# Optimization experiments

Measured on AMD Instinct MI355X. Metric: run time of the kernel, lower is better.

## Reference

```python
import jax, jax.numpy as jnp
import numpy as np

B, IN, H, N_FRAMES = 256, 1024, 2048, 32
BN_EPS = 1e-5


def setup_inputs() -> dict:
    key = jax.random.key(0)
    ks = jax.random.split(key, 10)
    s_in = 1.0 / np.sqrt(IN)
    s_h = 1.0 / np.sqrt(H)
    return {
        "x": jax.random.normal(ks[0], (B, IN), jnp.float32),
        "W_x": jax.random.normal(ks[1], (IN, 3 * H), jnp.float32) * s_in,
        "W_h": jax.random.normal(ks[2], (H, 3 * H), jnp.float32) * s_h,
        "b_x": jnp.zeros((3 * H,), jnp.float32),
        "b_h": jnp.zeros((3 * H,), jnp.float32),
        "W_d": jax.random.normal(ks[3], (H, IN), jnp.float32) * s_h,
        "b_d": jnp.zeros((IN,), jnp.float32),
        "gamma": jnp.ones((IN,), jnp.float32),
        "beta": jnp.zeros((IN,), jnp.float32),
        "n_frames": N_FRAMES,
    }


def reference(x, W_x, W_h, b_x, b_h, W_d, b_d, gamma, beta, n_frames):
    Bsz = x.shape[0]
    Hh = W_h.shape[0]
    h0 = jnp.zeros((Bsz, Hh), x.dtype)

    def step(carry, _):
        h, inp = carry
        gx = inp @ W_x + b_x                      # [B, 3H]
        gh = h @ W_h + b_h                        # [B, 3H]
        xr, xz, xn = jnp.split(gx, 3, axis=-1)
        hr, hz, hn = jnp.split(gh, 3, axis=-1)
        r = jax.nn.sigmoid(xr + hr)
        z = jax.nn.sigmoid(xz + hz)
        n = jnp.tanh(xn + r * hn)
        h_new = (1.0 - z) * n + z * h             # GRU update
        out = h_new @ W_d + b_d                   # fed back as next input
        return (h_new, out), out

    _, outs = jax.lax.scan(step, (h0, x), None, length=n_frames)  # [T, B, IN]
    # BatchNorm1d applied per frame over the batch dim (training-mode stats)
    mean = jnp.mean(outs, axis=1, keepdims=True)
    var = jnp.var(outs, axis=1, keepdims=True)
    return (outs - mean) * jax.lax.rsqrt(var + BN_EPS) * gamma + beta
```

## Files before the change

### kernel.cpp

```cpp
#include <hip/hip_runtime.h>
#include <hip/hip_bf16.h>
#include <stdint.h>


typedef __attribute__((ext_vector_type(8))) _Float16 half8;
typedef __attribute__((ext_vector_type(4))) float f32x4;
typedef unsigned short u16;

#define GLB_CAST(p) ((const __attribute__((address_space(1))) void*)(p))
#define LDS_CAST(p) ((__attribute__((address_space(3))) void*)(p))

static __device__ __forceinline__ void gload_lds16(const void* g, void* l) {
  __builtin_amdgcn_global_load_lds(GLB_CAST(g), LDS_CAST(l), 16, 0, 0);
}
static __device__ __forceinline__ u16 f2h(float f) {
  _Float16 h = (_Float16)f;
  return __builtin_bit_cast(u16, h);
}
static __device__ __forceinline__ float h2f(u16 u) {
  _Float16 h = __builtin_bit_cast(_Float16, u);
  return (float)h;
}

__global__ __launch_bounds__(256) void transpose_conv(
    const float* __restrict__ src, int src_ld, int j0,
    u16* __restrict__ dst, int dst_ld)
{
  __shared__ float tile[32][33];
  const int kt = blockIdx.y * 32, jt = blockIdx.x * 32;
  const int tr = threadIdx.x >> 5, tc = threadIdx.x & 31;
#pragma unroll
  for (int r = 0; r < 4; r++)
    tile[tr + r * 8][tc] = src[(size_t)(kt + tr + r * 8) * src_ld + j0 + jt + tc];
  __syncthreads();
#pragma unroll
  for (int r = 0; r < 4; r++)
    dst[(size_t)(jt + tr + r * 8) * dst_ld + kt + tc] = f2h(tile[tc][tr + r * 8]);
}

__global__ __launch_bounds__(256) void convert_f2h(
    const float* __restrict__ src, u16* __restrict__ dst)
{
  const int i = (blockIdx.x * 256 + threadIdx.x) * 4;
  float4 v = *(const float4*)(src + i);
  dst[i + 0] = f2h(v.x); dst[i + 1] = f2h(v.y);
  dst[i + 2] = f2h(v.z); dst[i + 3] = f2h(v.w);
}

__global__ __launch_bounds__(256) void bconst_kernel(
    const float* __restrict__ bx, const float* __restrict__ bd,
    const u16* __restrict__ XT, float* __restrict__ bc)
{
  __shared__ float sbd[1024];
  const int tid = threadIdx.x;
  for (int i = tid; i < 1024; i += 256) sbd[i] = bd[i];
  __syncthreads();
  const int j = blockIdx.x * 256 + tid;
  const u16* row = XT + (size_t)j * 1024;
  float s = bx[j];
  for (int k = 0; k < 1024; k += 8) {
    half8 v = *(const half8*)(row + k);
#pragma unroll
    for (int u = 0; u < 8; u++) s += sbd[k + u] * (float)v[u];
  }
  bc[j] = s;
}

template <int EPI>
__global__ __launch_bounds__(256) void gemm128_kernel(
    const u16* __restrict__ A, int lda,
    const u16* __restrict__ Bm, int ldb,
    int K, int ldc,
    u16* __restrict__ Cw, const u16* __restrict__ HT,
    float* __restrict__ Cf, const float* __restrict__ bias)
{
  __shared__ __attribute__((aligned(16))) u16 a_lds[128 * 64];
  __shared__ __attribute__((aligned(16))) u16 b_lds[128 * 64];
  const int tid = threadIdx.x, w = tid >> 6, l = tid & 63;
  const int rw = w >> 1, jw = w & 1;
  const int m0 = blockIdx.x * 128, n0 = blockIdx.y * 128;

  f32x4 acc[4][4] = {};

  for (int kk = 0; kk < K; kk += 64) {
    __syncthreads();
#pragma unroll
    for (int rnd = 0; rnd < 4; rnd++) {
      int flat = rnd * 256 + tid;
      int row = flat >> 3, gch = (flat & 7) ^ (row & 7);
      gload_lds16(A + (size_t)(m0 + row) * lda + kk + gch * 8, a_lds + flat * 8);
      gload_lds16(Bm + (size_t)(n0 + row) * ldb + kk + gch * 8, b_lds + flat * 8);
    }
    __syncthreads();
#pragma unroll
    for (int kh = 0; kh < 2; kh++) {
      const int koff = kh * 4 + (l >> 4);
      half8 a[4], b[4];
#pragma unroll
      for (int mf = 0; mf < 4; mf++) {
        int arow = rw * 64 + mf * 16 + (l & 15);
        a[mf] = *(const half8*)(a_lds + (arow * 8 + (koff ^ (arow & 7))) * 8);
      }
#pragma unroll
      for (int nf = 0; nf < 4; nf++) {
        int brow = jw * 64 + nf * 16 + (l & 15);
        b[nf] = *(const half8*)(b_lds + (brow * 8 + (koff ^ (brow & 7))) * 8);
      }
#pragma unroll
      for (int mf = 0; mf < 4; mf++)
#pragma unroll
        for (int nf = 0; nf < 4; nf++)
          acc[mf][nf] = __builtin_amdgcn_mfma_f32_16x16x32_f16(a[mf], b[nf], acc[mf][nf], 0, 0, 0);
    }
  }

#pragma unroll
  for (int mf = 0; mf < 4; mf++)
#pragma unroll
    for (int nf = 0; nf < 4; nf++) {
      const int n = n0 + jw * 64 + nf * 16 + (l & 15);
#pragma unroll
      for (int i = 0; i < 4; i++) {
        const int m = m0 + rw * 64 + mf * 16 + (l >> 4) * 4 + i;
        float v = acc[mf][nf][i];
        if (EPI == 0) {
          if (m < 4096) v += h2f(HT[(size_t)m * 2048 + n]);
          Cw[(size_t)m * ldc + n] = f2h(v);
        } else {
          Cf[(size_t)m * ldc + n] = v + bias[n];
        }
      }
    }
}

__global__ __launch_bounds__(512) void frame0_kernel(
    const u16* __restrict__ x16, const u16* __restrict__ XT,
    const float* __restrict__ bx, const float* __restrict__ bh,
    float* __restrict__ h32out, u16* __restrict__ hout16)
{
  __shared__ __attribute__((aligned(16))) u16 a_lds[2][64 * 64];
  __shared__ __attribute__((aligned(16))) u16 b_lds[2][96 * 64];
  const int tid = threadIdx.x, w = tid >> 6, l = tid & 63;
  const int rw = w >> 1, jw = w & 1;
  const int jt = blockIdx.x, r0 = blockIdx.y * 64;
  f32x4 acc[3] = {};

  const int ar = tid >> 3;
  const int agch = (tid & 7) ^ (ar & 7);
  const u16* asrc = x16 + (size_t)(r0 + ar) * 1024 + agch * 8;
  const u16* bsrc0;
  const u16* bsrc1;
  {
    int row0 = tid >> 3, gch0 = (tid & 7) ^ (row0 & 7);
    bsrc0 = XT + (size_t)((row0 >> 5) * 2048 + jt * 32 + (row0 & 31)) * 1024 + gch0 * 8;
    int flat = 512 + tid;
    int row1 = flat >> 3, gch1 = (flat & 7) ^ (row1 & 7);
    bsrc1 = XT + (size_t)((row1 >> 5) * 2048 + jt * 32 + (row1 & 31)) * 1024 + gch1 * 8;
  }

  auto stage = [&](int buf, int kk) {
    gload_lds16(asrc + kk, a_lds[buf] + tid * 8);
    gload_lds16(bsrc0 + kk, b_lds[buf] + tid * 8);
    if (512 + tid < 768)
      gload_lds16(bsrc1 + kk, b_lds[buf] + (512 + tid) * 8);
  };

  stage(0, 0);
  __syncthreads();
  int cur = 0;
  for (int t = 0; t < 16; ++t) {
    if (t < 15) stage(cur ^ 1, (t + 1) * 64);
    const int arow = rw * 16 + (l & 15);
#pragma unroll
    for (int kh = 0; kh < 2; kh++) {
      int apch = (kh * 4 + (l >> 4)) ^ (arow & 7);
      half8 a = *(const half8*)(a_lds[cur] + arow * 64 + apch * 8);
#pragma unroll
      for (int s = 0; s < 3; s++) {
        int brow = s * 32 + jw * 16 + (l & 15);
        int bpch = (kh * 4 + (l >> 4)) ^ (brow & 7);
        half8 bf = *(const half8*)(b_lds[cur] + brow * 64 + bpch * 8);
        acc[s] = __builtin_amdgcn_mfma_f32_16x16x32_f16(a, bf, acc[s], 0, 0, 0);
      }
    }
    __syncthreads();
    cur ^= 1;
  }

  const int j = jt * 32 + jw * 16 + (l & 15);
  const float cR = bx[j] + bh[j];
  const float cZ = bx[2048 + j] + bh[2048 + j];
  const float cX = bx[4096 + j];
  const float hn0 = bh[4096 + j];
#pragma unroll
  for (int i = 0; i < 4; i++) {
    const int b = r0 + rw * 16 + (l >> 4) * 4 + i;
    float r = 1.f / (1.f + __expf(-(acc[0][i] + cR)));
    float z = 1.f / (1.f + __expf(-(acc[1][i] + cZ)));
    float n = tanhf(acc[2][i] + cX + r * hn0);
    float hv = (1.f - z) * n;
    h32out[b * 2048 + j] = hv;
    hout16[b * 2048 + j] = f2h(hv);
  }
}

__global__ __launch_bounds__(512) void frame_kernel(
    const u16* __restrict__ hin16,
    const u16* __restrict__ WC,
    const float* __restrict__ bc, const float* __restrict__ bh,
    const float* __restrict__ h32in, float* __restrict__ h32out,
    u16* __restrict__ hout16)
{
  __shared__ __attribute__((aligned(16))) u16 a_lds[4][64 * 64];
  __shared__ __attribute__((aligned(16))) u16 b_lds[4][128 * 64];
  const int tid = threadIdx.x, w = tid >> 6, l = tid & 63;
  const int rw = (w >> 2) & 1, jw = (w >> 1) & 1, kw = w & 1;
  const int jt = blockIdx.x, r0 = blockIdx.y * 64;

  f32x4 acc[2][4] = {};

  const int ar = tid >> 3, agch = (tid & 7) ^ (ar & 7);
  const u16* asrc = hin16 + (size_t)(r0 + ar) * 2048 + agch * 8;
  const u16* bsrc0;
  const u16* bsrc1;
  {
    int row0 = tid >> 3, gch0 = (tid & 7) ^ (row0 & 7);
    bsrc0 = WC + (size_t)((row0 >> 5) * 2048 + jt * 32 + (row0 & 31)) * 2048 + gch0 * 8;
    int flat = 512 + tid;
    int row1 = flat >> 3, gch1 = (flat & 7) ^ (row1 & 7);
    bsrc1 = WC + (size_t)((row1 >> 5) * 2048 + jt * 32 + (row1 & 31)) * 2048 + gch1 * 8;
  }

  auto stage = [&](int buf, int step) {
    const int kk = step * 64;
    gload_lds16(asrc + kk, a_lds[buf] + tid * 8);
    gload_lds16(bsrc0 + kk, b_lds[buf] + tid * 8);
    gload_lds16(bsrc1 + kk, b_lds[buf] + (512 + tid) * 8);
  };

  auto compute = [&](int buf) {
    const int koff = kw * 4 + (l >> 4);
    half8 a[2], b[4];
#pragma unroll
    for (int mf = 0; mf < 2; mf++) {
      int arow = rw * 32 + mf * 16 + (l & 15);
      a[mf] = *(const half8*)(a_lds[buf] + (arow * 8 + (koff ^ (arow & 7))) * 8);
    }
#pragma unroll
    for (int s = 0; s < 4; s++) {
      int brow = s * 32 + jw * 16 + (l & 15);
      b[s] = *(const half8*)(b_lds[buf] + (brow * 8 + (koff ^ (brow & 7))) * 8);
    }
    __builtin_amdgcn_s_setprio(1);
#pragma unroll
    for (int mf = 0; mf < 2; mf++)
#pragma unroll
      for (int s = 0; s < 4; s++)
        acc[mf][s] = __builtin_amdgcn_mfma_f32_16x16x32_f16(a[mf], b[s], acc[mf][s], 0, 0, 0);
    __builtin_amdgcn_s_setprio(0);
  };

  stage(0, 0);
  stage(1, 1);
#pragma unroll 1
  for (int t = 0; t < 30; ++t) {
    stage((t + 2) & 3, t + 2);
    asm volatile("s_waitcnt vmcnt(6)\n\ts_barrier" ::: "memory");
    compute(t & 3);
  }
  asm volatile("s_waitcnt vmcnt(3)\n\ts_barrier" ::: "memory");
  compute(30 & 3);
  asm volatile("s_waitcnt vmcnt(0)\n\ts_barrier" ::: "memory");
  compute(31 & 3);

  __syncthreads();
  float* xch = (float*)&a_lds[0][0];
  const int wid2 = rw * 2 + jw;
  if (kw == 1) {
#pragma unroll
    for (int mf = 0; mf < 2; mf++)
#pragma unroll
      for (int s = 0; s < 4; s++)
        *(f32x4*)(xch + ((((wid2 * 2 + mf) * 4 + s) * 64 + l) * 4)) = acc[mf][s];
  }
  __syncthreads();
  if (kw == 0) {
#pragma unroll
    for (int mf = 0; mf < 2; mf++)
#pragma unroll
      for (int s = 0; s < 4; s++) {
        f32x4 p = *(const f32x4*)(xch + ((((wid2 * 2 + mf) * 4 + s) * 64 + l) * 4));
        acc[mf][s] += p;
      }
    const int j = jt * 32 + jw * 16 + (l & 15);
    const float cR = bc[j] + bh[j];
    const float cZ = bc[2048 + j] + bh[2048 + j];
    const float cX = bc[4096 + j];
    const float cH = bh[4096 + j];
#pragma unroll
    for (int mf = 0; mf < 2; mf++)
#pragma unroll
      for (int i = 0; i < 4; i++) {
        const int b = r0 + rw * 32 + mf * 16 + (l >> 4) * 4 + i;
        float r = 1.f / (1.f + __expf(-(acc[mf][0][i] + cR)));
        float z = 1.f / (1.f + __expf(-(acc[mf][1][i] + cZ)));
        float n = tanhf(acc[mf][2][i] + cX + r * (acc[mf][3][i] + cH));
        float hp = h32in[b * 2048 + j];
        float hv = (1.f - z) * n + z * hp;
        h32out[b * 2048 + j] = hv;
        hout16[b * 2048 + j] = f2h(hv);
      }
  }
}

__global__ __launch_bounds__(256) void bn_kernel(
    float* __restrict__ O, const float* __restrict__ gamma,
    const float* __restrict__ beta)
{
  const int t = blockIdx.x, j = blockIdx.y * 256 + threadIdx.x;
  const size_t base = (size_t)t * 256 * 1024 + j;
  float s = 0.f, q = 0.f;
  for (int b = 0; b < 256; b++) {
    float v = O[base + (size_t)b * 1024];
    s += v; q += v * v;
  }
  const float mean = s * (1.f / 256.f);
  const float var = q * (1.f / 256.f) - mean * mean;
  const float inv = rsqrtf(var + 1e-5f);
  const float g = gamma[j] * inv, be = beta[j];
  for (int b = 0; b < 256; b++) {
    const size_t idx = base + (size_t)b * 1024;
    O[idx] = (O[idx] - mean) * g + be;
  }
}

extern "C" void kernel_launch(void* const* d_in, const int* in_sizes, int n_in,
                              void* d_out, int out_size, void* d_ws, size_t ws_size,
                              hipStream_t stream)
{
  (void)in_sizes; (void)n_in; (void)out_size; (void)ws_size;
  const float* x  = (const float*)d_in[0];
  const float* Wx = (const float*)d_in[1];
  const float* Wh = (const float*)d_in[2];
  const float* bx = (const float*)d_in[3];
  const float* bh = (const float*)d_in[4];
  const float* Wd = (const float*)d_in[5];
  const float* bd = (const float*)d_in[6];
  const float* gamma = (const float*)d_in[7];
  const float* beta  = (const float*)d_in[8];

  char* p = (char*)d_ws;
  u16* XT  = (u16*)p;  p += (size_t)6144 * 1024 * 2;
  u16* WC  = (u16*)p;  p += (size_t)8192 * 2048 * 2;
  u16* DT  = (u16*)p;  p += (size_t)1024 * 2048 * 2;
  float* h32a = (float*)p; p += (size_t)256 * 2048 * 4;
  float* h32b = (float*)p; p += (size_t)256 * 2048 * 4;
  u16* x16 = (u16*)p;  p += (size_t)256 * 1024 * 2;
  float* bc = (float*)p; p += (size_t)6144 * 4;
  u16* Hs   = (u16*)p;
  u16* HT   = (u16*)p;
  u16* Wd16 = (u16*)(p + (size_t)4096 * 2048 * 2);

  const size_t BH = (size_t)256 * 2048;

  transpose_conv<<<dim3(192, 32), 256, 0, stream>>>(Wx, 6144, 0, XT, 1024);
  transpose_conv<<<dim3(128, 64), 256, 0, stream>>>(Wh, 6144, 0, HT, 2048);
  transpose_conv<<<dim3(64, 64), 256, 0, stream>>>(Wh, 6144, 4096,
                                                   WC + (size_t)6144 * 2048, 2048);
  transpose_conv<<<dim3(32, 64), 256, 0, stream>>>(Wd, 1024, 0, DT, 2048);
  convert_f2h<<<2048, 256, 0, stream>>>(Wd, Wd16);
  convert_f2h<<<256, 256, 0, stream>>>(x, x16);
  bconst_kernel<<<24, 256, 0, stream>>>(bx, bd, XT, bc);
  gemm128_kernel<0><<<dim3(48, 16), 256, 0, stream>>>(
      XT, 1024, Wd16, 1024, 1024, 2048, WC, HT, nullptr, nullptr);

  frame0_kernel<<<dim3(64, 4), 512, 0, stream>>>(x16, XT, bx, bh, h32a, Hs);
  for (int t = 1; t < 32; t++) {
    const float* hin32 = (t & 1) ? h32a : h32b;
    float* hout32      = (t & 1) ? h32b : h32a;
    frame_kernel<<<dim3(64, 4), 512, 0, stream>>>(
        Hs + (size_t)(t - 1) * BH, WC, bc, bh, hin32, hout32, Hs + (size_t)t * BH);
  }

  gemm128_kernel<1><<<dim3(64, 8), 256, 0, stream>>>(
      Hs, 2048, DT, 2048, 2048, 1024, nullptr, nullptr, (float*)d_out, bd);
  bn_kernel<<<dim3(32, 4), 256, 0, stream>>>((float*)d_out, gamma, beta);
}
```

Before: 810.7 us.

## Double-buffer GEMMs, widen frame K-step, fuse BN stats into output GEMM

The generic gemm128 kernel is split into two specialised 512-thread kernels, each with double-buffered LDS staging driven by explicit vmcnt waits. The output GEMM uses a wider 256-column tile and accumulates per-frame BatchNorm sum and sum-of-squares through shuffles and atomics, so the BN pass only reads the output once to normalise it. The recurrent frame kernel moves from a 4-deep 64-wide K pipeline to a 2-deep 128-wide K pipeline, halving the loop trip count and the number of barriers. The cost is larger LDS footprint and float atomics whose summation order is not deterministic.

Result: slower. 879.2 us (+8.4%).

```diff
diff --git a/kernel.cpp b/kernel.cpp
--- a/kernel.cpp
+++ b/kernel.cpp
@@ -66,45 +66,134 @@
   bc[j] = s;
 }
 
-template <int EPI>
-__global__ __launch_bounds__(256) void gemm128_kernel(
-    const u16* __restrict__ A, int lda,
-    const u16* __restrict__ Bm, int ldb,
-    int K, int ldc,
-    u16* __restrict__ Cw, const u16* __restrict__ HT,
-    float* __restrict__ Cf, const float* __restrict__ bias)
-{
-  __shared__ __attribute__((aligned(16))) u16 a_lds[128 * 64];
-  __shared__ __attribute__((aligned(16))) u16 b_lds[128 * 64];
+__global__ __launch_bounds__(512) void gemm_wc(
+    const u16* __restrict__ A, const u16* __restrict__ Bm,
+    const u16* __restrict__ HT, u16* __restrict__ Cw)
+{
+  __shared__ __attribute__((aligned(16))) u16 a_lds[2][128 * 64];
+  __shared__ __attribute__((aligned(16))) u16 b_lds[2][128 * 64];
   const int tid = threadIdx.x, w = tid >> 6, l = tid & 63;
   const int rw = w >> 1, jw = w & 1;
   const int m0 = blockIdx.x * 128, n0 = blockIdx.y * 128;
-
+  f32x4 acc[2][4] = {};
+
+  const u16 *asrc[2], *bsrc[2];
+#pragma unroll
+  for (int rnd = 0; rnd < 2; rnd++) {
+    int flat = rnd * 512 + tid;
+    int row = flat >> 3, gch = (flat & 7) ^ (row & 7);
+    asrc[rnd] = A + (size_t)(m0 + row) * 1024 + gch * 8;
+    bsrc[rnd] = Bm + (size_t)(n0 + row) * 1024 + gch * 8;
+  }
+  auto stage = [&](int buf, int kk) {
+#pragma unroll
+    for (int rnd = 0; rnd < 2; rnd++) {
+      int flat = rnd * 512 + tid;
+      gload_lds16(asrc[rnd] + kk, a_lds[buf] + flat * 8);
+      gload_lds16(bsrc[rnd] + kk, b_lds[buf] + flat * 8);
+    }
+  };
+  auto compute = [&](int buf) {
+    __builtin_amdgcn_s_setprio(1);
+#pragma unroll
+    for (int kh = 0; kh < 2; kh++) {
+      const int c = kh * 4 + (l >> 4);
+      half8 a[2], b[4];
+#pragma unroll
+      for (int mf = 0; mf < 2; mf++) {
+        int arow = rw * 32 + mf * 16 + (l & 15);
+        a[mf] = *(const half8*)(a_lds[buf] + (arow * 8 + (c ^ (arow & 7))) * 8);
+      }
+#pragma unroll
+      for (int nf = 0; nf < 4; nf++) {
+        int brow = jw * 64 + nf * 16 + (l & 15);
+        b[nf] = *(const half8*)(b_lds[buf] + (brow * 8 + (c ^ (brow & 7))) * 8);
+      }
+#pragma unroll
+      for (int mf = 0; mf < 2; mf++)
+#pragma unroll
+        for (int nf = 0; nf < 4; nf++)
+          acc[mf][nf] = __builtin_amdgcn_mfma_f32_16x16x32_f16(a[mf], b[nf], acc[mf][nf], 0, 0, 0);
+    }
+    __builtin_amdgcn_s_setprio(0);
+  };
+
+  stage(0, 0);
+#pragma unroll 1
+  for (int t = 0; t < 16; ++t) {
+    if (t < 15) {
+      stage((t + 1) & 1, (t + 1) * 64);
+      asm volatile("s_waitcnt vmcnt(4)\ns_barrier" ::: "memory");
+    } else {
+      asm volatile("s_waitcnt vmcnt(0)\ns_barrier" ::: "memory");
+    }
+    compute(t & 1);
+    asm volatile("s_barrier" ::: "memory");
+  }
+
+#pragma unroll
+  for (int mf = 0; mf < 2; mf++)
+#pragma unroll
+    for (int nf = 0; nf < 4; nf++) {
+      const int n = n0 + jw * 64 + nf * 16 + (l & 15);
+#pragma unroll
+      for (int i = 0; i < 4; i++) {
+        const int m = m0 + rw * 32 + mf * 16 + (l >> 4) * 4 + i;
+        float v = acc[mf][nf][i];
+        if (m < 4096) v += h2f(HT[(size_t)m * 2048 + n]);
+        Cw[(size_t)m * 2048 + n] = f2h(v);
+      }
+    }
+}
+
+__global__ __launch_bounds__(512) void gemm_out(
+    const u16* __restrict__ A, const u16* __restrict__ Bm,
+    const float* __restrict__ bd, float* __restrict__ O,
+    float* __restrict__ bnsum, float* __restrict__ bnsq)
+{
+  __shared__ __attribute__((aligned(16))) u16 a_lds[2][128 * 64];
+  __shared__ __attribute__((aligned(16))) u16 b_lds[2][256 * 64];
+  const int tid = threadIdx.x, w = tid >> 6, l = tid & 63;
+  const int rw = w >> 2, jw = w & 3;
+  const int m0 = blockIdx.x * 128, n0 = blockIdx.y * 256;
   f32x4 acc[4][4] = {};
 
-  for (int kk = 0; kk < K; kk += 64) {
-    __syncthreads();
-#pragma unroll
-    for (int rnd = 0; rnd < 4; rnd++) {
-      int flat = rnd * 256 + tid;
-      int row = flat >> 3, gch = (flat & 7) ^ (row & 7);
-      gload_lds16(A + (size_t)(m0 + row) * lda + kk + gch * 8, a_lds + flat * 8);
-      gload_lds16(Bm + (size_t)(n0 + row) * ldb + kk + gch * 8, b_lds + flat * 8);
-    }
-    __syncthreads();
+  const u16 *asrc[2], *bsrc[4];
+#pragma unroll
+  for (int rnd = 0; rnd < 2; rnd++) {
+    int flat = rnd * 512 + tid;
+    int row = flat >> 3, gch = (flat & 7) ^ (row & 7);
+    asrc[rnd] = A + (size_t)(m0 + row) * 2048 + gch * 8;
+  }
+#pragma unroll
+  for (int rnd = 0; rnd < 4; rnd++) {
+    int flat = rnd * 512 + tid;
+    int row = flat >> 3, gch = (flat & 7) ^ (row & 7);
+    bsrc[rnd] = Bm + (size_t)(n0 + row) * 2048 + gch * 8;
+  }
+  auto stage = [&](int buf, int kk) {
+#pragma unroll
+    for (int rnd = 0; rnd < 2; rnd++)
+      gload_lds16(asrc[rnd] + kk, a_lds[buf] + (rnd * 512 + tid) * 8);
+#pragma unroll
+    for (int rnd = 0; rnd < 4; rnd++)
+      gload_lds16(bsrc[rnd] + kk, b_lds[buf] + (rnd * 512 + tid) * 8);
+  };
+  auto compute = [&](int buf) {
+    __builtin_amdgcn_s_setprio(1);
 #pragma unroll
     for (int kh = 0; kh < 2; kh++) {
-      const int koff = kh * 4 + (l >> 4);
+      const int c = kh * 4 + (l >> 4);
       half8 a[4], b[4];
 #pragma unroll
       for (int mf = 0; mf < 4; mf++) {
         int arow = rw * 64 + mf * 16 + (l & 15);
-        a[mf] = *(const half8*)(a_lds + (arow * 8 + (koff ^ (arow & 7))) * 8);
+        a[mf] = *(const half8*)(a_lds[buf] + (arow * 8 + (c ^ (arow & 7))) * 8);
       }
 #pragma unroll
       for (int nf = 0; nf < 4; nf++) {
         int brow = jw * 64 + nf * 16 + (l & 15);
-        b[nf] = *(const half8*)(b_lds + (brow * 8 + (koff ^ (brow & 7))) * 8);
+        b[nf] = *(const half8*)(b_lds[buf] + (brow * 8 + (c ^ (brow & 7))) * 8);
       }
 #pragma unroll
       for (int mf = 0; mf < 4; mf++)
@@ -112,25 +201,44 @@
         for (int nf = 0; nf < 4; nf++)
           acc[mf][nf] = __builtin_amdgcn_mfma_f32_16x16x32_f16(a[mf], b[nf], acc[mf][nf], 0, 0, 0);
     }
-  }
-
-#pragma unroll
-  for (int mf = 0; mf < 4; mf++)
-#pragma unroll
-    for (int nf = 0; nf < 4; nf++) {
-      const int n = n0 + jw * 64 + nf * 16 + (l & 15);
+    __builtin_amdgcn_s_setprio(0);
+  };
+
+  stage(0, 0);
+#pragma unroll 1
+  for (int t = 0; t < 32; ++t) {
+    if (t < 31) {
+      stage((t + 1) & 1, (t + 1) * 64);
+      asm volatile("s_waitcnt vmcnt(6)\ns_barrier" ::: "memory");
+    } else {
+      asm volatile("s_waitcnt vmcnt(0)\ns_barrier" ::: "memory");
+    }
+    compute(t & 1);
+    asm volatile("s_barrier" ::: "memory");
+  }
+
+  const int fr = m0 >> 8;
+#pragma unroll
+  for (int nf = 0; nf < 4; nf++) {
+    const int n = n0 + jw * 64 + nf * 16 + (l & 15);
+    const float bb = bd[n];
+    float s = 0.f, q = 0.f;
+#pragma unroll
+    for (int mf = 0; mf < 4; mf++)
 #pragma unroll
       for (int i = 0; i < 4; i++) {
         const int m = m0 + rw * 64 + mf * 16 + (l >> 4) * 4 + i;
-        float v = acc[mf][nf][i];
-        if (EPI == 0) {
-          if (m < 4096) v += h2f(HT[(size_t)m * 2048 + n]);
-          Cw[(size_t)m * ldc + n] = f2h(v);
-        } else {
-          Cf[(size_t)m * ldc + n] = v + bias[n];
-        }
-      }
-    }
+        float v = acc[mf][nf][i] + bb;
+        O[(size_t)m * 1024 + n] = v;
+        s += v; q += v * v;
+      }
+    s += __shfl_xor(s, 16, 64); q += __shfl_xor(q, 16, 64);
+    s += __shfl_xor(s, 32, 64); q += __shfl_xor(q, 32, 64);
+    if (l < 16) {
+      atomicAdd(&bnsum[fr * 1024 + n], s);
+      atomicAdd(&bnsq[fr * 1024 + n], q);
+    }
+  }
 }
 
 __global__ __launch_bounds__(512) void frame0_kernel(
@@ -157,7 +265,6 @@
     int row1 = flat >> 3, gch1 = (flat & 7) ^ (row1 & 7);
     bsrc1 = XT + (size_t)((row1 >> 5) * 2048 + jt * 32 + (row1 & 31)) * 1024 + gch1 * 8;
   }
-
   auto stage = [&](int buf, int kk) {
     gload_lds16(asrc + kk, a_lds[buf] + tid * 8);
     gload_lds16(bsrc0 + kk, b_lds[buf] + tid * 8);
@@ -211,69 +318,75 @@
     const float* __restrict__ h32in, float* __restrict__ h32out,
     u16* __restrict__ hout16)
 {
-  __shared__ __attribute__((aligned(16))) u16 a_lds[4][64 * 64];
-  __shared__ __attribute__((aligned(16))) u16 b_lds[4][128 * 64];
+  __shared__ __attribute__((aligned(16))) u16 a_lds[2][64 * 128];
+  __shared__ __attribute__((aligned(16))) u16 b_lds[2][128 * 128];
   const int tid = threadIdx.x, w = tid >> 6, l = tid & 63;
   const int rw = (w >> 2) & 1, jw = (w >> 1) & 1, kw = w & 1;
   const int jt = blockIdx.x, r0 = blockIdx.y * 64;
 
   f32x4 acc[2][4] = {};
 
-  const int ar = tid >> 3, agch = (tid & 7) ^ (ar & 7);
-  const u16* asrc = hin16 + (size_t)(r0 + ar) * 2048 + agch * 8;
-  const u16* bsrc0;
-  const u16* bsrc1;
-  {
-    int row0 = tid >> 3, gch0 = (tid & 7) ^ (row0 & 7);
-    bsrc0 = WC + (size_t)((row0 >> 5) * 2048 + jt * 32 + (row0 & 31)) * 2048 + gch0 * 8;
-    int flat = 512 + tid;
-    int row1 = flat >> 3, gch1 = (flat & 7) ^ (row1 & 7);
-    bsrc1 = WC + (size_t)((row1 >> 5) * 2048 + jt * 32 + (row1 & 31)) * 2048 + gch1 * 8;
-  }
-
-  auto stage = [&](int buf, int step) {
-    const int kk = step * 64;
-    gload_lds16(asrc + kk, a_lds[buf] + tid * 8);
-    gload_lds16(bsrc0 + kk, b_lds[buf] + tid * 8);
-    gload_lds16(bsrc1 + kk, b_lds[buf] + (512 + tid) * 8);
-  };
-
+  const u16* asrc[2];
+  const u16* bsrc[4];
+#pragma unroll
+  for (int rnd = 0; rnd < 2; rnd++) {
+    int flat = rnd * 512 + tid;
+    int row = flat >> 4, gch = (flat & 15) ^ (row & 7);
+    asrc[rnd] = hin16 + (size_t)(r0 + row) * 2048 + gch * 8;
+  }
+#pragma unroll
+  for (int rnd = 0; rnd < 4; rnd++) {
+    int flat = rnd * 512 + tid;
+    int row = flat >> 4, gch = (flat & 15) ^ (row & 7);
+    int sec = row >> 5, jr = row & 31;
+    bsrc[rnd] = WC + (size_t)(sec * 2048 + jt * 32 + jr) * 2048 + gch * 8;
+  }
+  auto stage = [&](int buf, int kk) {
+#pragma unroll
+    for (int rnd = 0; rnd < 2; rnd++)
+      gload_lds16(asrc[rnd] + kk, a_lds[buf] + (rnd * 512 + tid) * 8);
+#pragma unroll
+    for (int rnd = 0; rnd < 4; rnd++)
+      gload_lds16(bsrc[rnd] + kk, b_lds[buf] + (rnd * 512 + tid) * 8);
+  };
   auto compute = [&](int buf) {
-    const int koff = kw * 4 + (l >> 4);
-    half8 a[2], b[4];
-#pragma unroll
-    for (int mf = 0; mf < 2; mf++) {
-      int arow = rw * 32 + mf * 16 + (l & 15);
-      a[mf] = *(const half8*)(a_lds[buf] + (arow * 8 + (koff ^ (arow & 7))) * 8);
-    }
-#pragma unroll
-    for (int s = 0; s < 4; s++) {
-      int brow = s * 32 + jw * 16 + (l & 15);
-      b[s] = *(const half8*)(b_lds[buf] + (brow * 8 + (koff ^ (brow & 7))) * 8);
-    }
     __builtin_amdgcn_s_setprio(1);
 #pragma unroll
-    for (int mf = 0; mf < 2; mf++)
-#pragma unroll
-      for (int s = 0; s < 4; s++)
-        acc[mf][s] = __builtin_amdgcn_mfma_f32_16x16x32_f16(a[mf], b[s], acc[mf][s], 0, 0, 0);
+    for (int kh = 0; kh < 2; kh++) {
+      const int c = kw * 8 + kh * 4 + (l >> 4);
+      half8 a[2], b[4];
+#pragma unroll
+      for (int mf = 0; mf < 2; mf++) {
+        int arow = rw * 32 + mf * 16 + (l & 15);
+        a[mf] = *(const half8*)(a_lds[buf] + (arow * 16 + (c ^ (arow & 7))) * 8);
+      }
+#pragma unroll
+      for (int s = 0; s < 4; s++) {
+        int brow = s * 32 + jw * 16 + (l & 15);
+        b[s] = *(const half8*)(b_lds[buf] + (brow * 16 + (c ^ (brow & 7))) * 8);
+      }
+#pragma unroll
+      for (int mf = 0; mf < 2; mf++)
+#pragma unroll
+        for (int s = 0; s < 4; s++)
+          acc[mf][s] = __builtin_amdgcn_mfma_f32_16x16x32_f16(a[mf], b[s], acc[mf][s], 0, 0, 0);
+    }
     __builtin_amdgcn_s_setprio(0);
   };
 
   stage(0, 0);
-  stage(1, 1);
 #pragma unroll 1
-  for (int t = 0; t < 30; ++t) {
-    stage((t + 2) & 3, t + 2);
-    asm volatile("s_waitcnt vmcnt(6)\n\ts_barrier" ::: "memory");
-    compute(t & 3);
-  }
-  asm volatile("s_waitcnt vmcnt(3)\n\ts_barrier" ::: "memory");
-  compute(30 & 3);
-  asm volatile("s_waitcnt vmcnt(0)\n\ts_barrier" ::: "memory");
-  compute(31 & 3);
-
-  __syncthreads();
+  for (int t = 0; t < 16; ++t) {
+    if (t < 15) {
+      stage((t + 1) & 1, (t + 1) * 128);
+      asm volatile("s_waitcnt vmcnt(6)\ns_barrier" ::: "memory");
+    } else {
+      asm volatile("s_waitcnt vmcnt(0)\ns_barrier" ::: "memory");
+    }
+    compute(t & 1);
+    asm volatile("s_barrier" ::: "memory");
+  }
+
   float* xch = (float*)&a_lds[0][0];
   const int wid2 = rw * 2 + jw;
   if (kw == 1) {
@@ -313,21 +426,17 @@
   }
 }
 
-__global__ __launch_bounds__(256) void bn_kernel(
-    float* __restrict__ O, const float* __restrict__ gamma,
+__global__ __launch_bounds__(256) void bn_apply(
+    float* __restrict__ O, const float* __restrict__ bnsum,
+    const float* __restrict__ bnsq, const float* __restrict__ gamma,
     const float* __restrict__ beta)
 {
   const int t = blockIdx.x, j = blockIdx.y * 256 + threadIdx.x;
-  const size_t base = (size_t)t * 256 * 1024 + j;
-  float s = 0.f, q = 0.f;
-  for (int b = 0; b < 256; b++) {
-    float v = O[base + (size_t)b * 1024];
-    s += v; q += v * v;
-  }
-  const float mean = s * (1.f / 256.f);
-  const float var = q * (1.f / 256.f) - mean * mean;
+  const float mean = bnsum[t * 1024 + j] * (1.f / 256.f);
+  const float var = bnsq[t * 1024 + j] * (1.f / 256.f) - mean * mean;
   const float inv = rsqrtf(var + 1e-5f);
   const float g = gamma[j] * inv, be = beta[j];
+  const size_t base = (size_t)t * 256 * 1024 + j;
   for (int b = 0; b < 256; b++) {
     const size_t idx = base + (size_t)b * 1024;
     O[idx] = (O[idx] - mean) * g + be;
@@ -357,6 +466,8 @@
   float* h32b = (float*)p; p += (size_t)256 * 2048 * 4;
   u16* x16 = (u16*)p;  p += (size_t)256 * 1024 * 2;
   float* bc = (float*)p; p += (size_t)6144 * 4;
+  float* bnsum = (float*)p; p += (size_t)32 * 1024 * 4;
+  float* bnsq  = (float*)p; p += (size_t)32 * 1024 * 4;
   u16* Hs   = (u16*)p;
   u16* HT   = (u16*)p;
   u16* Wd16 = (u16*)(p + (size_t)4096 * 2048 * 2);
@@ -371,8 +482,8 @@
   convert_f2h<<<2048, 256, 0, stream>>>(Wd, Wd16);
   convert_f2h<<<256, 256, 0, stream>>>(x, x16);
   bconst_kernel<<<24, 256, 0, stream>>>(bx, bd, XT, bc);
-  gemm128_kernel<0><<<dim3(48, 16), 256, 0, stream>>>(
-      XT, 1024, Wd16, 1024, 1024, 2048, WC, HT, nullptr, nullptr);
+  hipMemsetAsync(bnsum, 0, (size_t)2 * 32 * 1024 * 4, stream);
+  gemm_wc<<<dim3(48, 16), 512, 0, stream>>>(XT, Wd16, HT, WC);
 
   frame0_kernel<<<dim3(64, 4), 512, 0, stream>>>(x16, XT, bx, bh, h32a, Hs);
   for (int t = 1; t < 32; t++) {
@@ -382,7 +493,6 @@
         Hs + (size_t)(t - 1) * BH, WC, bc, bh, hin32, hout32, Hs + (size_t)t * BH);
   }
 
-  gemm128_kernel<1><<<dim3(64, 8), 256, 0, stream>>>(
-      Hs, 2048, DT, 2048, 2048, 1024, nullptr, nullptr, (float*)d_out, bd);
-  bn_kernel<<<dim3(32, 4), 256, 0, stream>>>((float*)d_out, gamma, beta);
-}
+  gemm_out<<<dim3(64, 4), 512, 0, stream>>>(Hs, DT, bd, (float*)d_out, bnsum, bnsq);
+  bn_apply<<<dim3(32, 4), 256, 0, stream>>>((float*)d_out, bnsum, bnsq, gamma, beta);
+}
```
